# Optimization experiments

Hardware: AMD Instinct MI355X
Metric: run time of the kernel (lower is better)

## Reference

```python
import jax, jax.numpy as jnp
import numpy as np

N_NODES = 50000
N_HEDGES = 5000
NNZ = 800000
IN_C = 128
D1 = 256
D2 = D1 // 4  # 64


def setup_inputs() -> dict:
    key = jax.random.key(0)
    ks = jax.random.split(key, 7)
    x = jax.random.normal(ks[0], (N_NODES, IN_C), dtype=jnp.float32)
    node_idx = jax.random.randint(ks[1], (NNZ,), 0, N_NODES, dtype=jnp.int32)
    hedge_idx = jax.random.randint(ks[2], (NNZ,), 0, N_HEDGES, dtype=jnp.int32)
    edge = jnp.stack([node_idx, hedge_idx], axis=0)  # [2, nnz]
    W1 = jax.random.normal(ks[3], (IN_C, D1), dtype=jnp.float32) / np.float32(np.sqrt(IN_C))
    b1 = jnp.zeros((D1,), dtype=jnp.float32)
    W2 = jax.random.normal(ks[4], (D1, D2), dtype=jnp.float32) / np.float32(np.sqrt(D1))
    b2 = jnp.zeros((D2,), dtype=jnp.float32)
    return {"x": x, "edge": edge, "W1": W1, "b1": b1, "W2": W2, "b2": b2}


def _hconv(x, W, b, node_idx, hedge_idx):
    # HypergraphConv (no attention, unit hyperedge weights):
    # out = D^{-1} H B^{-1} H^T (X W) + b
    xw = x @ W  # [N, F]
    ones = jnp.ones((node_idx.shape[0],), dtype=xw.dtype)
    deg = jax.ops.segment_sum(ones, node_idx, num_segments=N_NODES)      # D_i
    Dinv = jnp.where(deg > 0, 1.0 / deg, 0.0)
    cnt = jax.ops.segment_sum(ones, hedge_idx, num_segments=N_HEDGES)    # B_e
    Binv = jnp.where(cnt > 0, 1.0 / cnt, 0.0)
    # node -> hyperedge aggregation (gather + segment_sum), normalized by B^{-1}
    e = jax.ops.segment_sum(xw[node_idx], hedge_idx, num_segments=N_HEDGES) * Binv[:, None]
    # hyperedge -> node aggregation, normalized by D^{-1}
    out = jax.ops.segment_sum(e[hedge_idx], node_idx, num_segments=N_NODES) * Dinv[:, None]
    return out + b


def reference(x, edge, W1, b1, W2, b2):
    node_idx, hedge_idx = edge[0], edge[1]
    h = jax.nn.relu(_hconv(x, W1, b1, node_idx, hedge_idx))
    out = jax.nn.relu(_hconv(h, W2, b2, node_idx, hedge_idx))
    return out
```

## Files before the change

### kernel.cpp

```cpp
#include <hip/hip_runtime.h>

#define N_NODES 50000
#define N_HEDGES 5000
#define NNZ 800000
#define IN_C 128
#define D1 256
#define D2 64
#define SN 64
#define SH 256

#define DUMN 50000
#define DUMH 5000

#define HBK 20
#define NHB 250
#define HCAP 4096
#define NBK 100
#define NNB 500
#define NCAP 2048
#define BKT_BLOCKS ((NNZ + 2047) / 2048)

typedef unsigned int u32;
typedef unsigned short u16;
typedef __attribute__((ext_vector_type(8))) short short8;
typedef __attribute__((ext_vector_type(4))) float f32x4;

__device__ __forceinline__ float bf_lo(u32 u) { return __uint_as_float(u << 16); }
__device__ __forceinline__ float bf_hi(u32 u) { return __uint_as_float(u & 0xffff0000u); }
__device__ __forceinline__ u32 rne16(float f) {
    u32 u = __float_as_uint(f);
    return (u + 0x7fffu + ((u >> 16) & 1u)) >> 16;
}
__device__ __forceinline__ u32 pack2(float a, float b) {
    return rne16(a) | (rne16(b) << 16);
}
__device__ __forceinline__ void acc8(float* a, uint4 v) {
    a[0] += bf_lo(v.x); a[1] += bf_hi(v.x);
    a[2] += bf_lo(v.y); a[3] += bf_hi(v.y);
    a[4] += bf_lo(v.z); a[5] += bf_hi(v.z);
    a[6] += bf_lo(v.w); a[7] += bf_hi(v.w);
}

__global__ void cast_bucket(const float4* __restrict__ x, uint2* __restrict__ xb,
                            const float* __restrict__ W1, u16* __restrict__ w1hi,
                            u16* __restrict__ w1lo,
                            const float* __restrict__ W2, u16* __restrict__ w2hi,
                            u16* __restrict__ w2lo,
                            const int* __restrict__ nidx, const int* __restrict__ hidx,
                            int* __restrict__ gcur_h, int* __restrict__ gcur_n,
                            u32* __restrict__ pairs_h, u32* __restrict__ pairs_n,
                            uint4* __restrict__ xbz, uint4* __restrict__ aggz,
                            uint4* __restrict__ hwz, uint4* __restrict__ e2z) {
    __shared__ int hist_h[NHB], hist_n[NNB];
    __shared__ int base_h[NHB], base_n[NNB];
    int tid = threadIdx.x;
    int i = blockIdx.x * 256 + tid;
    float4 v = x[i];
    uint2 o;
    o.x = pack2(v.x, v.y);
    o.y = pack2(v.z, v.w);
    xb[i] = o;
    if (i < 32768) {
        int j = i & 7;
        int l = (i >> 3) & 63;
        int ct = (i >> 9) & 15;
        int kc = i >> 13;
        int k = kc * 32 + (l >> 4) * 8 + j;
        int n = ct * 16 + (l & 15);
        float w = W1[k * D1 + n];
        u32 h = rne16(w);
        w1hi[i] = (u16)h;
        w1lo[i] = (u16)rne16(w - bf_lo(h));
    } else if (i < 32768 + 16384) {
        int t = i - 32768;
        int j = t & 7;
        int l = (t >> 3) & 63;
        int nt = (t >> 9) & 3;
        int kc = t >> 11;
        int k = kc * 32 + (l >> 4) * 8 + j;
        int n = nt * 16 + (l & 15);
        float w = W2[k * D2 + n];
        u32 h = rne16(w);
        w2hi[t] = (u16)h;
        w2lo[t] = (u16)rne16(w - bf_lo(h));
    }
    if (blockIdx.x == gridDim.x - 1) {
        uint4 z = make_uint4(0u, 0u, 0u, 0u);
        if (tid < 16) xbz[tid] = z;
        else if (tid < 32) aggz[tid - 16] = z;
        else if (tid < 40) hwz[tid - 32] = z;
        else if (tid < 48) e2z[tid - 40] = z;
    }
    if (blockIdx.x >= BKT_BLOCKS) return;
    for (int t = tid; t < NHB; t += 256) hist_h[t] = 0;
    for (int t = tid; t < NNB; t += 256) hist_n[t] = 0;
    __syncthreads();
    int e0 = blockIdx.x * 2048 + tid * 8;
    int ns[8], hs_[8];
#pragma unroll
    for (int k = 0; k < 8; k++) {
        int e = e0 + k;
        if (e < NNZ) {
            ns[k] = nidx[e];
            hs_[k] = hidx[e];
            atomicAdd(&hist_h[hs_[k] / HBK], 1);
            atomicAdd(&hist_n[ns[k] / NBK], 1);
        } else {
            ns[k] = -1;
        }
    }
    __syncthreads();
    if (tid < NHB) base_h[tid] = atomicAdd(&gcur_h[tid], hist_h[tid]);
    for (int t = tid; t < NNB; t += 256) base_n[t] = atomicAdd(&gcur_n[t], hist_n[t]);
    __syncthreads();
    for (int t = tid; t < NHB; t += 256) hist_h[t] = 0;
    for (int t = tid; t < NNB; t += 256) hist_n[t] = 0;
    __syncthreads();
#pragma unroll
    for (int k = 0; k < 8; k++) {
        if (ns[k] >= 0) {
            int n = ns[k], h = hs_[k];
            int bh = h / HBK, bn = n / NBK;
            int s1 = base_h[bh] + atomicAdd(&hist_h[bh], 1);
            if (s1 < HCAP) pairs_h[bh * HCAP + s1] = ((u32)h << 16) | (u32)n;
            int s2 = base_n[bn] + atomicAdd(&hist_n[bn], 1);
            if (s2 < NCAP) pairs_n[bn * NCAP + s2] = ((u32)n << 16) | (u32)h;
        }
    }
}

__global__ void build_adj(const u32* __restrict__ pairs_h, const int* __restrict__ gcur_h,
                          u16* __restrict__ adj_h, int* __restrict__ cur_h,
                          const u32* __restrict__ pairs_n, const int* __restrict__ gcur_n,
                          u16* __restrict__ adj_n, int* __restrict__ cur_n) {
    __shared__ u16 rows[NBK * SN];
    __shared__ int cnt[NBK];
    int tid = threadIdx.x;
    if (blockIdx.x < NHB) {
        int b = blockIdx.x;
        if (tid < HBK) cnt[tid] = 0;
        {
            u32* rw = (u32*)rows;
            for (int t = tid; t < HBK * SH / 2; t += 256) rw[t] = (DUMN << 16) | DUMN;
        }
        __syncthreads();
        int np = gcur_h[b];
        if (np > HCAP) np = HCAP;
        for (int t = tid; t < np; t += 256) {
            u32 p = pairs_h[b * HCAP + t];
            int hl = (int)(p >> 16) - b * HBK;
            int s = atomicAdd(&cnt[hl], 1);
            if (s < SH) rows[hl * SH + s] = (u16)(p & 0xffff);
        }
        __syncthreads();
        u32* dst = (u32*)(adj_h + b * HBK * SH);
        const u32* srcl = (const u32*)rows;
        for (int t = tid; t < HBK * SH / 2; t += 256) dst[t] = srcl[t];
        if (tid < HBK) cur_h[b * HBK + tid] = cnt[tid];
    } else {
        int b = blockIdx.x - NHB;
        if (tid < NBK) cnt[tid] = 0;
        {
            u32* rw = (u32*)rows;
            for (int t = tid; t < NBK * SN / 2; t += 256) rw[t] = (DUMH << 16) | DUMH;
        }
        __syncthreads();
        int np = gcur_n[b];
        if (np > NCAP) np = NCAP;
        for (int t = tid; t < np; t += 256) {
            u32 p = pairs_n[b * NCAP + t];
            int nl = (int)(p >> 16) - b * NBK;
            int s = atomicAdd(&cnt[nl], 1);
            if (s < SN) rows[nl * SN + s] = (u16)(p & 0xffff);
        }
        __syncthreads();
        u32* dst = (u32*)(adj_n + b * NBK * SN);
        const u32* srcl = (const u32*)rows;
        for (int t = tid; t < NBK * SN / 2; t += 256) dst[t] = srcl[t];
        if (tid < NBK) cur_n[b * NBK + tid] = cnt[tid];
    }
}

template <int L>
__device__ __forceinline__ void gcore(const uint4* __restrict__ src,
                                      const u16* __restrict__ arow,
                                      int js, int je, int c,
                                      float* a0, float* a1, float* a2, float* a3) {
    if (js >= je) return;
    uint4 aa = *(const uint4*)(arow + js);
    for (int j = js; j < je; j += 8) {
        uint4 nx = aa;
        if (j + 8 < je) nx = *(const uint4*)(arow + j + 8);
        int i0 = aa.x & 0xffff, i1 = aa.x >> 16;
        int i2 = aa.y & 0xffff, i3 = aa.y >> 16;
        int i4 = aa.z & 0xffff, i5 = aa.z >> 16;
        int i6 = aa.w & 0xffff, i7 = aa.w >> 16;
        uint4 v0 = src[i0 * L + c];
        uint4 v1 = src[i1 * L + c];
        uint4 v2 = src[i2 * L + c];
        uint4 v3 = src[i3 * L + c];
        uint4 v4 = src[i4 * L + c];
        uint4 v5 = src[i5 * L + c];
        uint4 v6 = src[i6 * L + c];
        uint4 v7 = src[i7 * L + c];
        acc8(a0, v0); acc8(a1, v1); acc8(a2, v2); acc8(a3, v3);
        acc8(a0, v4); acc8(a1, v5); acc8(a2, v6); acc8(a3, v7);
        aa = nx;
    }
}

template <int F, int S, int SPLIT>
__global__ __launch_bounds__(256, 2)
void gather_split(const uint4* __restrict__ src, const int* __restrict__ cur,
                  const u16* __restrict__ adj, uint4* __restrict__ dst,
                  int nrows) {
    constexpr int L = F / 8;
    constexpr int TR = L * SPLIT;
    constexpr int RB = 256 / TR;
    constexpr int CHUNK = S / SPLIT;
    int tid = threadIdx.x;
    int rl = tid / TR;
    int seg = (tid % TR) / L;
    int c = tid % L;
    int row = blockIdx.x * RB + rl;
    bool valid = row < nrows;
    int len = valid ? cur[row] : 0;
    int lenc = (len < S) ? len : S;
    int lenp = (lenc + 7) & ~7;
    int js = seg * CHUNK;
    int je = (lenp < js + CHUNK) ? lenp : (js + CHUNK);
    float a0[8] = {0,0,0,0,0,0,0,0}, a1[8] = {0,0,0,0,0,0,0,0};
    float a2[8] = {0,0,0,0,0,0,0,0}, a3[8] = {0,0,0,0,0,0,0,0};
    if (valid)
        gcore<L>(src, adj + row * S, js, je, c, a0, a1, a2, a3);
    __shared__ float partf[256][8];
#pragma unroll
    for (int t = 0; t < 8; t++) partf[tid][t] = ((a0[t] + a1[t]) + (a2[t] + a3[t]));
    __syncthreads();
    if (seg == 0 && valid) {
        float r[8];
#pragma unroll
        for (int t = 0; t < 8; t++) r[t] = partf[tid][t];
#pragma unroll
        for (int s2 = 1; s2 < SPLIT; s2++) {
#pragma unroll
            for (int t = 0; t < 8; t++) r[t] += partf[tid + s2 * L][t];
        }
        float inv = (len > 0) ? 1.f / (float)len : 0.f;
        uint4 o;
        o.x = pack2(r[0] * inv, r[1] * inv);
        o.y = pack2(r[2] * inv, r[3] * inv);
        o.z = pack2(r[4] * inv, r[5] * inv);
        o.w = pack2(r[6] * inv, r[7] * inv);
        dst[row * L + c] = o;
    }
}

template <int F, int S, bool BIAS_RELU, bool DST_BF16>
__global__ __launch_bounds__(256, 2)
void gatherb(const uint4* __restrict__ src, const int* __restrict__ cur,
             const u16* __restrict__ adj, const float4* __restrict__ bias,
             void* __restrict__ dst, int nrows) {
    constexpr int L = F / 8;
    int gid = blockIdx.x * 256 + threadIdx.x;
    int row = gid / L;
    if (row >= nrows) return;
    int c = gid - row * L;
    int len = cur[row];
    int lenc = (len < S) ? len : S;
    int lenp = (lenc + 7) & ~7;
    float a0[8] = {0,0,0,0,0,0,0,0}, a1[8] = {0,0,0,0,0,0,0,0};
    float a2[8] = {0,0,0,0,0,0,0,0}, a3[8] = {0,0,0,0,0,0,0,0};
    gcore<L>(src, adj + row * S, 0, lenp, c, a0, a1, a2, a3);
    float inv = (len > 0) ? 1.f / (float)len : 0.f;
    float r[8];
#pragma unroll
    for (int t = 0; t < 8; t++) r[t] = ((a0[t] + a1[t]) + (a2[t] + a3[t])) * inv;
    if (BIAS_RELU) {
        float4 b0 = bias[c * 2], b1v = bias[c * 2 + 1];
        r[0] = fmaxf(r[0] + b0.x, 0.f); r[1] = fmaxf(r[1] + b0.y, 0.f);
        r[2] = fmaxf(r[2] + b0.z, 0.f); r[3] = fmaxf(r[3] + b0.w, 0.f);
        r[4] = fmaxf(r[4] + b1v.x, 0.f); r[5] = fmaxf(r[5] + b1v.y, 0.f);
        r[6] = fmaxf(r[6] + b1v.z, 0.f); r[7] = fmaxf(r[7] + b1v.w, 0.f);
    }
    if (DST_BF16) {
        uint4 o;
        o.x = pack2(r[0], r[1]);
        o.y = pack2(r[2], r[3]);
        o.z = pack2(r[4], r[5]);
        o.w = pack2(r[6], r[7]);
        ((uint4*)dst)[row * L + c] = o;
    } else {
        float4* d = (float4*)dst;
        d[row * (F / 4) + c * 2]     = make_float4(r[0], r[1], r[2], r[3]);
        d[row * (F / 4) + c * 2 + 1] = make_float4(r[4], r[5], r[6], r[7]);
    }
}

#define HSTRIDE 264
__global__ __launch_bounds__(256, 3)
void mlp64(const u16* __restrict__ sb,
           const short8* __restrict__ w1hi, const short8* __restrict__ w1lo,
           const float* __restrict__ b1,
           const short8* __restrict__ w2hi, const short8* __restrict__ w2lo,
           u16* __restrict__ hw) {
    __shared__ u16 hs[64 * HSTRIDE];
    int tid = threadIdx.x;
    int node0 = blockIdx.x * 64;
    int wave = tid >> 6;
    int lane = tid & 63;
    int m = lane & 15;
    int q = lane >> 4;
    f32x4 acc[4][4];
#pragma unroll
    for (int i = 0; i < 4; i++) {
        float bc = b1[(wave * 4 + i) * 16 + m];
#pragma unroll
        for (int mt = 0; mt < 4; mt++)
            acc[i][mt] = (f32x4){bc, bc, bc, bc};
    }
#pragma unroll
    for (int kc = 0; kc < 4; kc++) {
        short8 am[4];
#pragma unroll
        for (int mt = 0; mt < 4; mt++)
            am[mt] = *(const short8*)&sb[(node0 + mt * 16 + m) * IN_C + kc * 32 + q * 8];
        short8 w[4];
#pragma unroll
        for (int i = 0; i < 4; i++)
            w[i] = w1hi[(kc * 16 + wave * 4 + i) * 64 + lane];
#pragma unroll
        for (int i = 0; i < 4; i++)
#pragma unroll
            for (int mt = 0; mt < 4; mt++)
                acc[i][mt] = __builtin_amdgcn_mfma_f32_16x16x32_bf16(am[mt], w[i], acc[i][mt], 0, 0, 0);
#pragma unroll
        for (int i = 0; i < 4; i++)
            w[i] = w1lo[(kc * 16 + wave * 4 + i) * 64 + lane];
#pragma unroll
        for (int i = 0; i < 4; i++)
#pragma unroll
            for (int mt = 0; mt < 4; mt++)
                acc[i][mt] = __builtin_amdgcn_mfma_f32_16x16x32_bf16(am[mt], w[i], acc[i][mt], 0, 0, 0);
    }
#pragma unroll
    for (int i = 0; i < 4; i++) {
        int col = (wave * 4 + i) * 16 + m;
#pragma unroll
        for (int mt = 0; mt < 4; mt++)
#pragma unroll
            for (int r = 0; r < 4; r++) {
                float h = fmaxf(acc[i][mt][r], 0.f);
                hs[(mt * 16 + q * 4 + r) * HSTRIDE + col] = (u16)rne16(h);
            }
    }
    __syncthreads();
    f32x4 acc2[4];
#pragma unroll
    for (int mt = 0; mt < 4; mt++) acc2[mt] = (f32x4){0.f, 0.f, 0.f, 0.f};
#pragma unroll
    for (int kc = 0; kc < 8; kc++) {
        short8 ah[4];
#pragma unroll
        for (int mt = 0; mt < 4; mt++)
            ah[mt] = *(const short8*)&hs[(mt * 16 + m) * HSTRIDE + kc * 32 + q * 8];
        short8 whi = w2hi[(kc * 4 + wave) * 64 + lane];
#pragma unroll
        for (int mt = 0; mt < 4; mt++)
            acc2[mt] = __builtin_amdgcn_mfma_f32_16x16x32_bf16(ah[mt], whi, acc2[mt], 0, 0, 0);
        short8 wlo = w2lo[(kc * 4 + wave) * 64 + lane];
#pragma unroll
        for (int mt = 0; mt < 4; mt++)
            acc2[mt] = __builtin_amdgcn_mfma_f32_16x16x32_bf16(ah[mt], wlo, acc2[mt], 0, 0, 0);
    }
#pragma unroll
    for (int mt = 0; mt < 4; mt++)
#pragma unroll
        for (int r = 0; r < 4; r++) {
            int row = node0 + mt * 16 + q * 4 + r;
            if (row < N_NODES)
                hw[row * D2 + wave * 16 + m] = (u16)rne16(acc2[mt][r]);
        }
}

extern "C" void kernel_launch(void* const* d_in, const int* in_sizes, int n_in,
                              void* d_out, int out_size, void* d_ws, size_t ws_size,
                              hipStream_t stream) {
    const float* x  = (const float*)d_in[0];
    const int* edge = (const int*)d_in[1];
    const int* nidx = edge;
    const int* hidx = edge + NNZ;
    const float* W1 = (const float*)d_in[2];
    const float* b1 = (const float*)d_in[3];
    const float* W2 = (const float*)d_in[4];
    const float* b2 = (const float*)d_in[5];
    float* out = (float*)d_out;

    u16* xb     = (u16*)d_ws;
    u16* aggxb  = xb + (N_NODES + 1) * IN_C;
    u16* hwb    = aggxb + (N_HEDGES + 1) * IN_C;
    u16* e2b    = hwb + (N_NODES + 1) * D2;
    u16* w1hi   = e2b + (N_HEDGES + 1) * D2;
    u16* w1lo   = w1hi + 32768;
    u16* w2hi   = w1lo + 32768;
    u16* w2lo   = w2hi + 16384;
    u16* adj_n  = w2lo + 16384;
    u16* adj_h  = adj_n + N_NODES * SN;
    u32* pairs_h = (u32*)(adj_h + N_HEDGES * SH);
    u32* pairs_n = pairs_h + NHB * HCAP;
    int* cur_n  = (int*)(pairs_n + NNB * NCAP);
    int* cur_h  = cur_n + N_NODES;
    int* gcur_h = cur_h + N_HEDGES;
    int* gcur_n = gcur_h + 256;
    u16* sb     = (u16*)(gcur_n + 512);

    hipMemsetAsync(gcur_h, 0, (256 + 512) * sizeof(int), stream);

    cast_bucket<<<N_NODES * IN_C / 4 / 256, 256, 0, stream>>>(
        (const float4*)x, (uint2*)xb, W1, w1hi, w1lo, W2, w2hi, w2lo,
        nidx, hidx, gcur_h, gcur_n, pairs_h, pairs_n,
        (uint4*)(xb + DUMN * IN_C), (uint4*)(aggxb + DUMH * IN_C),
        (uint4*)(hwb + DUMN * D2), (uint4*)(e2b + DUMH * D2));

    build_adj<<<NHB + NNB, 256, 0, stream>>>(pairs_h, gcur_h, adj_h, cur_h,
                                             pairs_n, gcur_n, adj_n, cur_n);

    gather_split<IN_C, SH, 4><<<(N_HEDGES + 3) / 4, 256, 0, stream>>>(
        (const uint4*)xb, cur_h, adj_h, (uint4*)aggxb, N_HEDGES);

    gatherb<IN_C, SN, false, true><<<(N_NODES * (IN_C / 8) + 255) / 256, 256, 0, stream>>>(
        (const uint4*)aggxb, cur_n, adj_n, (const float4*)b1, (void*)sb, N_NODES);

    mlp64<<<(N_NODES + 63) / 64, 256, 0, stream>>>(
        sb, (const short8*)w1hi, (const short8*)w1lo, b1,
        (const short8*)w2hi, (const short8*)w2lo, hwb);

    gather_split<D2, SH, 8><<<(N_HEDGES + 3) / 4, 256, 0, stream>>>(
        (const uint4*)hwb, cur_h, adj_h, (uint4*)e2b, N_HEDGES);
    gatherb<D2, SN, true, false><<<(N_NODES * (D2 / 8) + 255) / 256, 256, 0, stream>>>(
        (const uint4*)e2b, cur_n, adj_n, (const float4*)b2, out, N_NODES);
}
```

Measured before the change: 201.7 us.

## Replace hyperedge gather with LDS double-buffered async global_load_lds kernel

Adds a new hyperedge aggregation kernel that stages neighbor rows into shared memory with global_load_lds, double-buffering chunks of 16 neighbors per wave and reducing across lane groups with shuffles. It replaces the split-register gather for the first layer's node-to-hyperedge step. The aim is to overlap memory fetches with accumulation and raise outstanding loads per wave. It relies on manual vmcnt waits and reads padded indices beyond len (dummy rows), and it uses more LDS, which can limit occupancy.

```diff
diff --git a/kernel.cpp b/kernel.cpp
--- a/kernel.cpp
+++ b/kernel.cpp
@@ -24,6 +24,9 @@
 typedef unsigned short u16;
 typedef __attribute__((ext_vector_type(8))) short short8;
 typedef __attribute__((ext_vector_type(4))) float f32x4;
+
+typedef __attribute__((address_space(3))) unsigned ldsU;
+typedef const __attribute__((address_space(1))) unsigned glbU;
 
 __device__ __forceinline__ float bf_lo(u32 u) { return __uint_as_float(u << 16); }
 __device__ __forceinline__ float bf_hi(u32 u) { return __uint_as_float(u & 0xffff0000u); }
@@ -209,6 +212,73 @@
     }
 }
 
+#define GHC 16
+__global__ __launch_bounds__(256, 2)
+void gather_hs(const u16* __restrict__ src, const int* __restrict__ cur,
+               const u16* __restrict__ adj, uint4* __restrict__ dst) {
+    __shared__ u16 sbuf[4][2][GHC * 128];
+    __shared__ u16 idxl[4][256];
+    int tid = threadIdx.x;
+    int wave = tid >> 6;
+    int lane = tid & 63;
+    int row = blockIdx.x * 4 + wave;
+    int len = cur[row];
+    int lenc = (len < SH) ? len : SH;
+    int nc = (lenc + GHC - 1) / GHC;
+    ((unsigned long long*)idxl[wave])[lane] =
+        ((const unsigned long long*)(adj + row * SH))[lane];
+    int c = lane & 15;
+    int g = lane >> 4;
+    float p[8] = {0, 0, 0, 0, 0, 0, 0, 0};
+    if (nc > 0) {
+#pragma unroll
+        for (int i = 0; i < 4; i++) {
+            int mi = idxl[wave][i * 4 + g];
+            const u16* gp = src + mi * 128 + c * 8;
+            __builtin_amdgcn_global_load_lds((glbU*)(const unsigned*)gp,
+                                             (ldsU*)(unsigned*)&sbuf[wave][0][i * 512],
+                                             16, 0, 0);
+        }
+        for (int k = 0; k < nc; k++) {
+            int b = k & 1;
+            if (k + 1 < nc) {
+#pragma unroll
+                for (int i = 0; i < 4; i++) {
+                    int mi = idxl[wave][(k + 1) * GHC + i * 4 + g];
+                    const u16* gp = src + mi * 128 + c * 8;
+                    __builtin_amdgcn_global_load_lds((glbU*)(const unsigned*)gp,
+                                                     (ldsU*)(unsigned*)&sbuf[wave][b ^ 1][i * 512],
+                                                     16, 0, 0);
+                }
+                asm volatile("s_waitcnt vmcnt(4)" ::: "memory");
+            } else {
+                asm volatile("s_waitcnt vmcnt(0)" ::: "memory");
+            }
+            const u16* sb = sbuf[wave][b];
+#pragma unroll
+            for (int t = 0; t < 4; t++) {
+                uint4 v = *(const uint4*)&sb[(g + 4 * t) * 128 + c * 8];
+                acc8(p, v);
+            }
+            asm volatile("" ::: "memory");
+        }
+    }
+#pragma unroll
+    for (int t = 0; t < 8; t++) {
+        p[t] += __shfl_xor(p[t], 16, 64);
+        p[t] += __shfl_xor(p[t], 32, 64);
+    }
+    float inv = (len > 0) ? 1.f / (float)len : 0.f;
+    if (lane < 16) {
+        uint4 o;
+        o.x = pack2(p[0] * inv, p[1] * inv);
+        o.y = pack2(p[2] * inv, p[3] * inv);
+        o.z = pack2(p[4] * inv, p[5] * inv);
+        o.w = pack2(p[6] * inv, p[7] * inv);
+        dst[row * 16 + c] = o;
+    }
+}
+
 template <int F, int S, int SPLIT>
 __global__ __launch_bounds__(256, 2)
 void gather_split(const uint4* __restrict__ src, const int* __restrict__ cur,
@@ -425,8 +495,7 @@
     build_adj<<<NHB + NNB, 256, 0, stream>>>(pairs_h, gcur_h, adj_h, cur_h,
                                              pairs_n, gcur_n, adj_n, cur_n);
 
-    gather_split<IN_C, SH, 4><<<(N_HEDGES + 3) / 4, 256, 0, stream>>>(
-        (const uint4*)xb, cur_h, adj_h, (uint4*)aggxb, N_HEDGES);
+    gather_hs<<<N_HEDGES / 4, 256, 0, stream>>>(xb, cur_h, adj_h, (uint4*)aggxb);
 
     gatherb<IN_C, SN, false, true><<<(N_NODES * (IN_C / 8) + 255) / 256, 256, 0, stream>>>(
         (const uint4*)aggxb, cur_n, adj_n, (const float4*)b1, (void*)sb, N_NODES);
```

Result: no change. 203.0 us (+0.6%).

## Stage hyperedge feature slices in LDS for node-side gather

Applied to the files above, without the earlier changes.

Hyperedge aggregates are now written channel-slice-major (transposed with stride PSTR), so each block of the node-side gather loads one 16-byte channel slice for all 5000 hyperedges into shared memory (about 80 KB) and serves its random gathers from LDS rather than global memory/L2. Each block then handles 1024 nodes for one channel slice, with a 2D grid over node chunks and slices. In exchange, the adjacency list is re-read once per slice, and the large LDS footprint limits occupancy to one block per CU. The global dummy rows are dropped because the padding entry is zeroed inside LDS instead.

```diff
diff --git a/kernel.cpp b/kernel.cpp
--- a/kernel.cpp
+++ b/kernel.cpp
@@ -8,6 +8,7 @@
 #define D2 64
 #define SN 64
 #define SH 256
+#define PSTR 5008
 
 #define DUMN 50000
 #define DUMH 5000
@@ -49,8 +50,7 @@
                             const int* __restrict__ nidx, const int* __restrict__ hidx,
                             int* __restrict__ gcur_h, int* __restrict__ gcur_n,
                             u32* __restrict__ pairs_h, u32* __restrict__ pairs_n,
-                            uint4* __restrict__ xbz, uint4* __restrict__ aggz,
-                            uint4* __restrict__ hwz, uint4* __restrict__ e2z) {
+                            uint4* __restrict__ xbz, uint4* __restrict__ hwz) {
     __shared__ int hist_h[NHB], hist_n[NNB];
     __shared__ int base_h[NHB], base_n[NNB];
     int tid = threadIdx.x;
@@ -87,9 +87,7 @@
     if (blockIdx.x == gridDim.x - 1) {
         uint4 z = make_uint4(0u, 0u, 0u, 0u);
         if (tid < 16) xbz[tid] = z;
-        else if (tid < 32) aggz[tid - 16] = z;
-        else if (tid < 40) hwz[tid - 32] = z;
-        else if (tid < 48) e2z[tid - 40] = z;
+        else if (tid < 24) hwz[tid - 16] = z;
     }
     if (blockIdx.x >= BKT_BLOCKS) return;
     for (int t = tid; t < NHB; t += 256) hist_h[t] = 0;
@@ -252,48 +250,70 @@
         o.y = pack2(r[2] * inv, r[3] * inv);
         o.z = pack2(r[4] * inv, r[5] * inv);
         o.w = pack2(r[6] * inv, r[7] * inv);
-        dst[row * L + c] = o;
-    }
-}
-
-template <int F, int S, bool BIAS_RELU, bool DST_BF16>
+        dst[c * PSTR + row] = o;
+    }
+}
+
+template <int NCH, bool BIAS_RELU, bool DST_F32>
 __global__ __launch_bounds__(256, 2)
-void gatherb(const uint4* __restrict__ src, const int* __restrict__ cur,
-             const u16* __restrict__ adj, const float4* __restrict__ bias,
-             void* __restrict__ dst, int nrows) {
-    constexpr int L = F / 8;
-    int gid = blockIdx.x * 256 + threadIdx.x;
-    int row = gid / L;
-    if (row >= nrows) return;
-    int c = gid - row * L;
-    int len = cur[row];
-    int lenc = (len < S) ? len : S;
-    int lenp = (lenc + 7) & ~7;
-    float a0[8] = {0,0,0,0,0,0,0,0}, a1[8] = {0,0,0,0,0,0,0,0};
-    float a2[8] = {0,0,0,0,0,0,0,0}, a3[8] = {0,0,0,0,0,0,0,0};
-    gcore<L>(src, adj + row * S, 0, lenp, c, a0, a1, a2, a3);
-    float inv = (len > 0) ? 1.f / (float)len : 0.f;
-    float r[8];
-#pragma unroll
-    for (int t = 0; t < 8; t++) r[t] = ((a0[t] + a1[t]) + (a2[t] + a3[t])) * inv;
+void gather_slice(const uint4* __restrict__ srcT, const int* __restrict__ cur,
+                  const u16* __restrict__ adj, const float* __restrict__ bias,
+                  void* __restrict__ dst) {
+    __shared__ uint4 plane[PSTR];
+    int tid = threadIdx.x;
+    int c = blockIdx.y;
+    const uint4* gp = srcT + c * PSTR;
+    for (int t = tid; t < N_HEDGES; t += 256) plane[t] = gp[t];
+    __syncthreads();
+    if (tid == 0) plane[DUMH] = make_uint4(0u, 0u, 0u, 0u);
+    __syncthreads();
+    float bb[8];
     if (BIAS_RELU) {
-        float4 b0 = bias[c * 2], b1v = bias[c * 2 + 1];
-        r[0] = fmaxf(r[0] + b0.x, 0.f); r[1] = fmaxf(r[1] + b0.y, 0.f);
-        r[2] = fmaxf(r[2] + b0.z, 0.f); r[3] = fmaxf(r[3] + b0.w, 0.f);
-        r[4] = fmaxf(r[4] + b1v.x, 0.f); r[5] = fmaxf(r[5] + b1v.y, 0.f);
-        r[6] = fmaxf(r[6] + b1v.z, 0.f); r[7] = fmaxf(r[7] + b1v.w, 0.f);
-    }
-    if (DST_BF16) {
-        uint4 o;
-        o.x = pack2(r[0], r[1]);
-        o.y = pack2(r[2], r[3]);
-        o.z = pack2(r[4], r[5]);
-        o.w = pack2(r[6], r[7]);
-        ((uint4*)dst)[row * L + c] = o;
-    } else {
-        float4* d = (float4*)dst;
-        d[row * (F / 4) + c * 2]     = make_float4(r[0], r[1], r[2], r[3]);
-        d[row * (F / 4) + c * 2 + 1] = make_float4(r[4], r[5], r[6], r[7]);
+#pragma unroll
+        for (int t = 0; t < 8; t++) bb[t] = bias[c * 8 + t];
+    }
+    int base = blockIdx.x * 1024;
+#pragma unroll 1
+    for (int i = 0; i < 4; i++) {
+        int node = base + i * 256 + tid;
+        if (node >= N_NODES) break;
+        int len = cur[node];
+        int lenc = (len < SN) ? len : SN;
+        int lenp = (lenc + 7) & ~7;
+        const u16* arow = adj + node * SN;
+        float a0[8] = {0,0,0,0,0,0,0,0}, a1[8] = {0,0,0,0,0,0,0,0};
+        float a2[8] = {0,0,0,0,0,0,0,0}, a3[8] = {0,0,0,0,0,0,0,0};
+        for (int j = 0; j < lenp; j += 8) {
+            uint4 aa = *(const uint4*)(arow + j);
+            acc8(a0, plane[aa.x & 0xffff]);
+            acc8(a1, plane[aa.x >> 16]);
+            acc8(a2, plane[aa.y & 0xffff]);
+            acc8(a3, plane[aa.y >> 16]);
+            acc8(a0, plane[aa.z & 0xffff]);
+            acc8(a1, plane[aa.z >> 16]);
+            acc8(a2, plane[aa.w & 0xffff]);
+            acc8(a3, plane[aa.w >> 16]);
+        }
+        float inv = (len > 0) ? 1.f / (float)len : 0.f;
+        float r[8];
+#pragma unroll
+        for (int t = 0; t < 8; t++) r[t] = ((a0[t] + a1[t]) + (a2[t] + a3[t])) * inv;
+        if (BIAS_RELU) {
+#pragma unroll
+            for (int t = 0; t < 8; t++) r[t] = fmaxf(r[t] + bb[t], 0.f);
+        }
+        if (DST_F32) {
+            float4* d = (float4*)((float*)dst + node * (NCH * 8) + c * 8);
+            d[0] = make_float4(r[0], r[1], r[2], r[3]);
+            d[1] = make_float4(r[4], r[5], r[6], r[7]);
+        } else {
+            uint4 o;
+            o.x = pack2(r[0], r[1]);
+            o.y = pack2(r[2], r[3]);
+            o.z = pack2(r[4], r[5]);
+            o.w = pack2(r[6], r[7]);
+            ((uint4*)dst)[node * NCH + c] = o;
+        }
     }
 }
 
@@ -397,10 +417,10 @@
     float* out = (float*)d_out;
 
     u16* xb     = (u16*)d_ws;
-    u16* aggxb  = xb + (N_NODES + 1) * IN_C;
-    u16* hwb    = aggxb + (N_HEDGES + 1) * IN_C;
-    u16* e2b    = hwb + (N_NODES + 1) * D2;
-    u16* w1hi   = e2b + (N_HEDGES + 1) * D2;
+    u16* aggxbT = xb + (N_NODES + 1) * IN_C;
+    u16* hwb    = aggxbT + 16 * PSTR * 8;
+    u16* e2bT   = hwb + (N_NODES + 1) * D2;
+    u16* w1hi   = e2bT + 8 * PSTR * 8;
     u16* w1lo   = w1hi + 32768;
     u16* w2hi   = w1lo + 32768;
     u16* w2lo   = w2hi + 16384;
@@ -419,24 +439,24 @@
     cast_bucket<<<N_NODES * IN_C / 4 / 256, 256, 0, stream>>>(
         (const float4*)x, (uint2*)xb, W1, w1hi, w1lo, W2, w2hi, w2lo,
         nidx, hidx, gcur_h, gcur_n, pairs_h, pairs_n,
-        (uint4*)(xb + DUMN * IN_C), (uint4*)(aggxb + DUMH * IN_C),
-        (uint4*)(hwb + DUMN * D2), (uint4*)(e2b + DUMH * D2));
+        (uint4*)(xb + DUMN * IN_C), (uint4*)(hwb + DUMN * D2));
 
     build_adj<<<NHB + NNB, 256, 0, stream>>>(pairs_h, gcur_h, adj_h, cur_h,
                                              pairs_n, gcur_n, adj_n, cur_n);
 
     gather_split<IN_C, SH, 4><<<(N_HEDGES + 3) / 4, 256, 0, stream>>>(
-        (const uint4*)xb, cur_h, adj_h, (uint4*)aggxb, N_HEDGES);
-
-    gatherb<IN_C, SN, false, true><<<(N_NODES * (IN_C / 8) + 255) / 256, 256, 0, stream>>>(
-        (const uint4*)aggxb, cur_n, adj_n, (const float4*)b1, (void*)sb, N_NODES);
+        (const uint4*)xb, cur_h, adj_h, (uint4*)aggxbT, N_HEDGES);
+
+    gather_slice<16, false, false><<<dim3((N_NODES + 1023) / 1024, 16), 256, 0, stream>>>(
+        (const uint4*)aggxbT, cur_n, adj_n, b1, (void*)sb);
 
     mlp64<<<(N_NODES + 63) / 64, 256, 0, stream>>>(
         sb, (const short8*)w1hi, (const short8*)w1lo, b1,
         (const short8*)w2hi, (const short8*)w2lo, hwb);
 
     gather_split<D2, SH, 8><<<(N_HEDGES + 3) / 4, 256, 0, stream>>>(
-        (const uint4*)hwb, cur_h, adj_h, (uint4*)e2b, N_HEDGES);
-    gatherb<D2, SN, true, false><<<(N_NODES * (D2 / 8) + 255) / 256, 256, 0, stream>>>(
-        (const uint4*)e2b, cur_n, adj_n, (const float4*)b2, out, N_NODES);
-}
+        (const uint4*)hwb, cur_h, adj_h, (uint4*)e2bT, N_HEDGES);
+
+    gather_slice<8, true, true><<<dim3((N_NODES + 1023) / 1024, 8), 256, 0, stream>>>(
+        (const uint4*)e2bT, cur_n, adj_n, b2, (void*)out);
+}
```

Result: slower. 236.9 us (+17.4%).
